# Optimization experiments

Hardware: AMD Instinct MI355X
Metric: run time of the kernel (lower is better)

## Reference

```python
import jax, jax.numpy as jnp
import numpy as np

N = 50000      # nodes
E = 800000     # edges
IN = 128       # in_size
H = 128        # hid_size
OUT = 40       # out_size
L = 3          # num_hid_layers
K = 32         # maxk


def _xavier(key, shape):
    fan_in, fan_out = shape[0], shape[1]
    limit = np.sqrt(6.0 / (fan_in + fan_out))
    return jax.random.uniform(key, shape, jnp.float32, -limit, limit)


def setup_inputs() -> dict:
    key = jax.random.key(0)
    ks = jax.random.split(key, 16)
    x = jax.random.normal(ks[0], (N, IN), jnp.float32)
    src = jax.random.randint(ks[1], (E,), 0, N, jnp.int32)
    dst = jax.random.randint(ks[2], (E,), 0, N, jnp.int32)
    # weights stored as [in, out] so forward is x @ W + b (math-equivalent to torch Linear)
    W_in = _xavier(ks[3], (IN, H)); b_in = jnp.zeros((H,), jnp.float32)
    W_lin = jnp.stack([_xavier(jax.random.fold_in(ks[4], i), (H, H)) for i in range(L)])
    b_lin = jnp.zeros((L, H), jnp.float32)
    W1 = jnp.stack([_xavier(jax.random.fold_in(ks[5], i), (H, H)) for i in range(L)])
    b1 = jnp.zeros((L, H), jnp.float32)
    W2 = jnp.stack([_xavier(jax.random.fold_in(ks[6], i), (H, H)) for i in range(L)])
    b2 = jnp.zeros((L, H), jnp.float32)
    eps = jnp.zeros((L,), jnp.float32)  # learnable eps, init 0
    W_out = _xavier(ks[7], (H, OUT)); b_out = jnp.zeros((OUT,), jnp.float32)
    return {"x": x, "src": src, "dst": dst, "W_in": W_in, "b_in": b_in,
            "W_lin": W_lin, "b_lin": b_lin, "W1": W1, "b1": b1,
            "W2": W2, "b2": b2, "eps": eps, "W_out": W_out, "b_out": b_out}


def _maxk(h, k):
    # keep top-k entries per row, zero the rest (threshold form; ties negligible for random floats)
    thr = jax.lax.top_k(h, k)[0][:, -1:]  # [N, 1] kth-largest value
    return jnp.where(h >= thr, h, 0.0)


def reference(x, src, dst, W_in, b_in, W_lin, b_lin, W1, b1, W2, b2, eps, W_out, b_out):
    h = jax.nn.relu(x @ W_in + b_in)  # [N, H]
    for i in range(L):
        h = h @ W_lin[i] + b_lin[i]
        # GIN conv with MaxK sparsified messages (dropout p=0 / eval mode)
        hs = _maxk(h, K)                                             # [N, H] top-K sparse
        neigh = jax.ops.segment_sum(hs[src], dst, num_segments=N)    # copy_u + sum
        o = (1.0 + eps[i]) * h + neigh
        h = jax.nn.relu(o @ W1[i] + b1[i]) @ W2[i] + b2[i]
    return h @ W_out + b_out  # [N, OUT]
```

## Files before the change

### kernel.cpp

```cpp
#include <hip/hip_runtime.h>

typedef __bf16 bf16x8 __attribute__((ext_vector_type(8)));
typedef float f32x4 __attribute__((ext_vector_type(4)));

__device__ inline unsigned short f2b(float f) {
  unsigned int u = __float_as_uint(f);
  u += 0x7fffu + ((u >> 16) & 1u);
  return (unsigned short)(u >> 16);
}
__device__ inline float b2f(unsigned short u) {
  return __uint_as_float(((unsigned int)u) << 16);
}

__device__ inline int swz(int r, int c) { return r * 128 + (c ^ ((r & 7) << 3)); }

__device__ inline bf16x8 ldfrag(const unsigned short* p) {
  uint4 v = *(const uint4*)p;
  bf16x8 r;
  __builtin_memcpy(&r, &v, 16);
  return r;
}

__global__ __launch_bounds__(256) void prep_wt(
    const float* __restrict__ W_in, const float* __restrict__ W_lin,
    const float* __restrict__ W1, const float* __restrict__ W2,
    const float* __restrict__ W_out, unsigned short* __restrict__ Wh,
    unsigned short* __restrict__ Wl)
{
  int slot = blockIdx.y;
  int e = blockIdx.x * 256 + threadIdx.x;
  int n = e >> 7, k = e & 127;
  const float* srcp; int N;
  if (slot == 0)      { srcp = W_in;                   N = 128; }
  else if (slot < 4)  { srcp = W_lin + (slot-1)*16384; N = 128; }
  else if (slot < 7)  { srcp = W1   + (slot-4)*16384;  N = 128; }
  else if (slot < 10) { srcp = W2   + (slot-7)*16384;  N = 128; }
  else                { srcp = W_out;                  N = 40;  }
  float v = (n < N) ? srcp[k * N + n] : 0.f;
  unsigned short hi = f2b(v);
  float lo = v - b2f(hi);
  Wh[slot * 16384 + e] = hi;
  Wl[slot * 16384 + e] = f2b(lo);
}

template<int WM, int WN, int MF, int NF, int AK, bool RELU>
__global__ __launch_bounds__(256) void gemm_k(
    const float* __restrict__ Ap, const float* __restrict__ neigh,
    const float* __restrict__ epsp, const unsigned short* __restrict__ Wh,
    const unsigned short* __restrict__ Wl, const float* __restrict__ bias,
    float* __restrict__ Cp, int M, int Ncols)
{
  constexpr int BM = WM * MF * 16;
  static_assert(BM * 128 % 1024 == 0, "");
  __shared__ __align__(16) unsigned short ldsAh[BM * 128];
  __shared__ __align__(16) unsigned short ldsAl[BM * 128];

  const int tid = threadIdx.x;
  const int row0 = blockIdx.x * BM;
  float epsf = 0.f;
  if constexpr (AK == 1) epsf = 1.0f + epsp[0];

  constexpr int AIT = BM * 128 / 1024;
#pragma unroll
  for (int it = 0; it < AIT; ++it) {
    int flat = it * 1024 + tid * 4;
    int r = flat >> 7, c = flat & 127;
    int gr = row0 + r;
    float4 v = make_float4(0.f, 0.f, 0.f, 0.f);
    if (gr < M) {
      v = *(const float4*)(Ap + (size_t)gr * 128 + c);
      if constexpr (AK == 1) {
        float4 ng = *(const float4*)(neigh + (size_t)gr * 128 + c);
        v = make_float4(fmaf(epsf, v.x, ng.x), fmaf(epsf, v.y, ng.y),
                        fmaf(epsf, v.z, ng.z), fmaf(epsf, v.w, ng.w));
      }
    }
    ushort4 h4, l4;
    h4.x = f2b(v.x); l4.x = f2b(v.x - b2f(h4.x));
    h4.y = f2b(v.y); l4.y = f2b(v.y - b2f(h4.y));
    h4.z = f2b(v.z); l4.z = f2b(v.z - b2f(h4.z));
    h4.w = f2b(v.w); l4.w = f2b(v.w - b2f(h4.w));
    *(ushort4*)&ldsAh[swz(r, c)] = h4;
    *(ushort4*)&ldsAl[swz(r, c)] = l4;
  }
  __syncthreads();

  const int wid = tid >> 6, lane = tid & 63;
  const int wm = wid / WN, wn = wid % WN;
  const int l15 = lane & 15, lk = lane >> 4;

  f32x4 acc[MF][NF];
#pragma unroll
  for (int mi = 0; mi < MF; ++mi)
#pragma unroll
    for (int ni = 0; ni < NF; ++ni)
      acc[mi][ni] = (f32x4){0.f, 0.f, 0.f, 0.f};

  const unsigned short* wbh = Wh + (size_t)(wn * NF * 16 + l15) * 128;
  const unsigned short* wbl = Wl + (size_t)(wn * NF * 16 + l15) * 128;

#pragma unroll
  for (int kk = 0; kk < 4; ++kk) {
    const int kc = kk * 32 + lk * 8;
    bf16x8 ah[MF], al[MF];
#pragma unroll
    for (int mi = 0; mi < MF; ++mi) {
      int rr = wm * MF * 16 + mi * 16 + l15;
      ah[mi] = ldfrag(&ldsAh[swz(rr, kc)]);
      al[mi] = ldfrag(&ldsAl[swz(rr, kc)]);
    }
    bf16x8 bh[NF], bl[NF];
#pragma unroll
    for (int ni = 0; ni < NF; ++ni) {
      bh[ni] = ldfrag(wbh + ni * 16 * 128 + kc);
      bl[ni] = ldfrag(wbl + ni * 16 * 128 + kc);
    }
#pragma unroll
    for (int mi = 0; mi < MF; ++mi)
#pragma unroll
      for (int ni = 0; ni < NF; ++ni) {
        acc[mi][ni] = __builtin_amdgcn_mfma_f32_16x16x32_bf16(ah[mi], bl[ni], acc[mi][ni], 0, 0, 0);
        acc[mi][ni] = __builtin_amdgcn_mfma_f32_16x16x32_bf16(al[mi], bh[ni], acc[mi][ni], 0, 0, 0);
        acc[mi][ni] = __builtin_amdgcn_mfma_f32_16x16x32_bf16(ah[mi], bh[ni], acc[mi][ni], 0, 0, 0);
      }
  }

#pragma unroll
  for (int ni = 0; ni < NF; ++ni) {
    int col = wn * NF * 16 + ni * 16 + l15;
    if (col >= Ncols) continue;
    float bc = bias[col];
#pragma unroll
    for (int mi = 0; mi < MF; ++mi) {
      int rbase = row0 + wm * MF * 16 + mi * 16 + lk * 4;
#pragma unroll
      for (int j = 0; j < 4; ++j) {
        int r = rbase + j;
        if (r >= M) continue;
        float v = acc[mi][ni][j] + bc;
        if (RELU) v = fmaxf(v, 0.f);
        Cp[(size_t)r * Ncols + col] = v;
      }
    }
  }
}

__global__ __launch_bounds__(256) void maxk_k(const float* __restrict__ h,
                                              float* __restrict__ hs, int M)
{
  int row = blockIdx.x * 4 + (threadIdx.x >> 6);
  if (row >= M) return;
  int lane = threadIdx.x & 63;
  float2 pr = *(const float2*)(h + (size_t)row * 128 + lane * 2);
  auto key = [](float f) -> unsigned int {
    unsigned int b = __float_as_uint(f);
    return (b & 0x80000000u) ? ~b : (b | 0x80000000u);
  };
  unsigned int k0 = key(pr.x), k1 = key(pr.y);
  unsigned int thr = 0;
#pragma unroll
  for (int b = 31; b >= 0; --b) {
    unsigned int t = thr | (1u << b);
    int c = __popcll(__ballot(k0 >= t)) + __popcll(__ballot(k1 >= t));
    if (c >= 32) thr = t;
  }
  unsigned long long g0 = __ballot(k0 > thr), g1 = __ballot(k1 > thr);
  unsigned long long e0 = __ballot(k0 == thr), e1 = __ballot(k1 == thr);
  int cgt = __popcll(g0) + __popcll(g1);
  unsigned long long mlt = (1ull << lane) - 1ull;
  unsigned long long mle = mlt | (1ull << lane);
  bool keep0 = (k0 > thr) ||
               ((k0 == thr) && (cgt + __popcll(e0 & mlt) + __popcll(e1 & mlt)) < 32);
  bool keep1 = (k1 > thr) ||
               ((k1 == thr) && (cgt + __popcll(e0 & mle) + __popcll(e1 & mlt)) < 32);
  float2 o;
  o.x = keep0 ? pr.x : 0.f;
  o.y = keep1 ? pr.y : 0.f;
  *(float2*)(hs + (size_t)row * 128 + lane * 2) = o;
}

__global__ __launch_bounds__(256) void hist_k(const int* __restrict__ dst,
                                              int* __restrict__ cnt, int E)
{
  int e = blockIdx.x * 256 + threadIdx.x;
  if (e < E) atomicAdd(&cnt[dst[e]], 1);
}

__global__ __launch_bounds__(256) void bsum_k(const int* __restrict__ cnt,
                                              int* __restrict__ bsum, int M)
{
  __shared__ int s[256];
  int i = blockIdx.x * 256 + threadIdx.x;
  int t = threadIdx.x;
  s[t] = (i < M) ? cnt[i] : 0;
  __syncthreads();
  for (int st = 128; st > 0; st >>= 1) {
    if (t < st) s[t] += s[t + st];
    __syncthreads();
  }
  if (t == 0) bsum[blockIdx.x] = s[0];
}

__global__ __launch_bounds__(1024) void scanb_k(int* __restrict__ bsum, int NB)
{
  __shared__ int s[1024];
  int t = threadIdx.x;
  int v = (t < NB) ? bsum[t] : 0;
  s[t] = v;
  __syncthreads();
  for (int st = 1; st < 1024; st <<= 1) {
    int a = (t >= st) ? s[t - st] : 0;
    __syncthreads();
    s[t] += a;
    __syncthreads();
  }
  if (t < NB) bsum[t] = s[t] - v;
}

__global__ __launch_bounds__(256) void scano_k(const int* __restrict__ cnt,
                                               const int* __restrict__ bsum,
                                               int* __restrict__ offs,
                                               int* __restrict__ cur, int M, int E)
{
  __shared__ int s[256];
  int i = blockIdx.x * 256 + threadIdx.x;
  int t = threadIdx.x;
  int v = (i < M) ? cnt[i] : 0;
  s[t] = v;
  __syncthreads();
  for (int st = 1; st < 256; st <<= 1) {
    int a = (t >= st) ? s[t - st] : 0;
    __syncthreads();
    s[t] += a;
    __syncthreads();
  }
  int excl = s[t] - v + bsum[blockIdx.x];
  if (i < M) { offs[i] = excl; cur[i] = excl; }
  if (blockIdx.x == 0 && t == 0) offs[M] = E;
}

__global__ __launch_bounds__(256) void fill_k(const int* __restrict__ src,
                                              const int* __restrict__ dst,
                                              int* __restrict__ cur,
                                              unsigned short* __restrict__ eidx, int E)
{
  int e = blockIdx.x * 256 + threadIdx.x;
  if (e >= E) return;
  int d = dst[e];
  int p = atomicAdd(&cur[d], 1);
  eidx[p] = (unsigned short)src[e];
}

__global__ __launch_bounds__(256) void gather_k(
    const float* __restrict__ hs, const int* __restrict__ offs,
    const unsigned short* __restrict__ eidx, float* __restrict__ neigh, int M)
{
  const int w = threadIdx.x >> 6, lane = threadIdx.x & 63;
  const int d = blockIdx.x * 4 + w;
  if (d >= M) return;
  const int start = offs[d], end = offs[d + 1];
  const size_t co = (size_t)lane * 2;
  float ax = 0.f, ay = 0.f;
  int i = start;
  for (; i + 4 <= end; i += 4) {
    int s0 = eidx[i], s1 = eidx[i + 1], s2 = eidx[i + 2], s3 = eidx[i + 3];
    float2 v0 = *(const float2*)(hs + (size_t)s0 * 128 + co);
    float2 v1 = *(const float2*)(hs + (size_t)s1 * 128 + co);
    float2 v2 = *(const float2*)(hs + (size_t)s2 * 128 + co);
    float2 v3 = *(const float2*)(hs + (size_t)s3 * 128 + co);
    ax += (v0.x + v1.x) + (v2.x + v3.x);
    ay += (v0.y + v1.y) + (v2.y + v3.y);
  }
  for (; i < end; ++i) {
    int s0 = eidx[i];
    float2 v0 = *(const float2*)(hs + (size_t)s0 * 128 + co);
    ax += v0.x;
    ay += v0.y;
  }
  float2 o;
  o.x = ax;
  o.y = ay;
  *(float2*)(neigh + (size_t)d * 128 + co) = o;
}

extern "C" void kernel_launch(void* const* d_in, const int* in_sizes, int n_in,
                              void* d_out, int out_size, void* d_ws, size_t ws_size,
                              hipStream_t stream)
{
  const float* x     = (const float*)d_in[0];
  const int*   src   = (const int*)d_in[1];
  const int*   dst   = (const int*)d_in[2];
  const float* W_in  = (const float*)d_in[3];
  const float* b_in  = (const float*)d_in[4];
  const float* W_lin = (const float*)d_in[5];
  const float* b_lin = (const float*)d_in[6];
  const float* W1    = (const float*)d_in[7];
  const float* b1    = (const float*)d_in[8];
  const float* W2    = (const float*)d_in[9];
  const float* b2    = (const float*)d_in[10];
  const float* eps   = (const float*)d_in[11];
  const float* W_out = (const float*)d_in[12];
  const float* b_out = (const float*)d_in[13];

  const int M = in_sizes[0] / 128;
  const int E = in_sizes[1];

  const int NB = (M + 255) / 256;
  char* ws = (char*)d_ws;
  unsigned short* Wh = (unsigned short*)ws;
  size_t off = (size_t)11 * 16384 * 2;
  unsigned short* Wl = (unsigned short*)(ws + off); off += (size_t)11 * 16384 * 2;
  float* PA    = (float*)(ws + off); off += (size_t)M * 128 * 4;
  float* PB    = (float*)(ws + off); off += (size_t)M * 128 * 4;
  float* neigh = (float*)(ws + off); off += (size_t)M * 128 * 4;
  int* offs = (int*)(ws + off); off += (size_t)(M + 1) * 4;
  unsigned short* eidx = (unsigned short*)(ws + off); off += (size_t)E * 2;
  int* cnt  = (int*)(ws + off); off += (size_t)M * 4;
  int* cur  = (int*)(ws + off); off += (size_t)M * 4;
  int* bsum = (int*)(ws + off); off += (size_t)NB * 4;

  dim3 blk(256);
  prep_wt<<<dim3(64, 11), blk, 0, stream>>>(W_in, W_lin, W1, W2, W_out, Wh, Wl);

  (void)hipMemsetAsync(cnt, 0, (size_t)M * 4, stream);
  hist_k<<<(E + 255) / 256, blk, 0, stream>>>(dst, cnt, E);
  bsum_k<<<NB, blk, 0, stream>>>(cnt, bsum, M);
  scanb_k<<<1, 1024, 0, stream>>>(bsum, NB);
  scano_k<<<NB, blk, 0, stream>>>(cnt, bsum, offs, cur, M, E);
  fill_k<<<(E + 255) / 256, blk, 0, stream>>>(src, dst, cur, eidx, E);

  const int gm = (M + 63) / 64;

  float* cur_h = PA;
  float* oth   = PB;
  gemm_k<2,2,2,4,0,true><<<gm, blk, 0, stream>>>(
      x, nullptr, nullptr, Wh, Wl, b_in, cur_h, M, 128);

  for (int i = 0; i < 3; ++i) {
    const size_t ws_off = (size_t)(1 + i) * 16384;
    gemm_k<2,2,2,4,0,false><<<gm, blk, 0, stream>>>(
        cur_h, nullptr, nullptr, Wh + ws_off, Wl + ws_off, b_lin + i * 128, oth, M, 128);
    float* hs = cur_h;
    maxk_k<<<(M + 3) / 4, blk, 0, stream>>>(oth, hs, M);
    gather_k<<<(M + 3) / 4, blk, 0, stream>>>(hs, offs, eidx, neigh, M);
    const size_t w1_off = (size_t)(4 + i) * 16384;
    gemm_k<2,2,2,4,1,true><<<gm, blk, 0, stream>>>(
        oth, neigh, eps + i, Wh + w1_off, Wl + w1_off, b1 + i * 128, cur_h, M, 128);
    const size_t w2_off = (size_t)(7 + i) * 16384;
    gemm_k<2,2,2,4,0,false><<<gm, blk, 0, stream>>>(
        cur_h, nullptr, nullptr, Wh + w2_off, Wl + w2_off, b2 + i * 128, oth, M, 128);
    float* t = cur_h; cur_h = oth; oth = t;
  }

  const size_t wo_off = (size_t)10 * 16384;
  gemm_k<4,1,1,3,0,false><<<gm, blk, 0, stream>>>(
      cur_h, nullptr, nullptr, Wh + wo_off, Wl + wo_off, b_out, (float*)d_out, M, 40);
}
```

Before: 698.8 us.

## Fuse GIN MLP GEMMs and store sparse messages as packed bf16

The two per-layer MLP GEMMs (W1 with ReLU, then W2) become one kernel that keeps the intermediate activation in LDS as hi/lo bf16 splits, so it is never written to and reread from global memory. Separately, maxk now writes the sparsified features as packed bf16 pairs, which halves the bytes the random-access gather reads per edge. The bf16 messages drop the split-precision accuracy that the GEMMs keep, which adds rounding error to the neighbour sums.

```diff
diff --git a/kernel.cpp b/kernel.cpp
--- a/kernel.cpp
+++ b/kernel.cpp
@@ -43,10 +43,9 @@
   Wl[slot * 16384 + e] = f2b(lo);
 }
 
-template<int WM, int WN, int MF, int NF, int AK, bool RELU>
+template<int WM, int WN, int MF, int NF, bool RELU>
 __global__ __launch_bounds__(256) void gemm_k(
-    const float* __restrict__ Ap, const float* __restrict__ neigh,
-    const float* __restrict__ epsp, const unsigned short* __restrict__ Wh,
+    const float* __restrict__ Ap, const unsigned short* __restrict__ Wh,
     const unsigned short* __restrict__ Wl, const float* __restrict__ bias,
     float* __restrict__ Cp, int M, int Ncols)
 {
@@ -57,8 +56,6 @@
 
   const int tid = threadIdx.x;
   const int row0 = blockIdx.x * BM;
-  float epsf = 0.f;
-  if constexpr (AK == 1) epsf = 1.0f + epsp[0];
 
   constexpr int AIT = BM * 128 / 1024;
 #pragma unroll
@@ -67,14 +64,7 @@
     int r = flat >> 7, c = flat & 127;
     int gr = row0 + r;
     float4 v = make_float4(0.f, 0.f, 0.f, 0.f);
-    if (gr < M) {
-      v = *(const float4*)(Ap + (size_t)gr * 128 + c);
-      if constexpr (AK == 1) {
-        float4 ng = *(const float4*)(neigh + (size_t)gr * 128 + c);
-        v = make_float4(fmaf(epsf, v.x, ng.x), fmaf(epsf, v.y, ng.y),
-                        fmaf(epsf, v.z, ng.z), fmaf(epsf, v.w, ng.w));
-      }
-    }
+    if (gr < M) v = *(const float4*)(Ap + (size_t)gr * 128 + c);
     ushort4 h4, l4;
     h4.x = f2b(v.x); l4.x = f2b(v.x - b2f(h4.x));
     h4.y = f2b(v.y); l4.y = f2b(v.y - b2f(h4.y));
@@ -145,8 +135,155 @@
   }
 }
 
+__global__ __launch_bounds__(256) void fusedgemm_k(
+    const float* __restrict__ h2, const float* __restrict__ neigh,
+    const float* __restrict__ epsp,
+    const unsigned short* __restrict__ Wh1, const unsigned short* __restrict__ Wl1,
+    const float* __restrict__ b1,
+    const unsigned short* __restrict__ Wh2, const unsigned short* __restrict__ Wl2,
+    const float* __restrict__ b2, float* __restrict__ Hout, int M)
+{
+  constexpr int WM = 2, WN = 2, MF = 2, NF = 4;
+  constexpr int BM = WM * MF * 16;
+  __shared__ __align__(16) unsigned short ldsAh[BM * 128];
+  __shared__ __align__(16) unsigned short ldsAl[BM * 128];
+
+  const int tid = threadIdx.x;
+  const int row0 = blockIdx.x * BM;
+  const float epsf = 1.0f + epsp[0];
+
+#pragma unroll
+  for (int it = 0; it < BM * 128 / 1024; ++it) {
+    int flat = it * 1024 + tid * 4;
+    int r = flat >> 7, c = flat & 127;
+    int gr = row0 + r;
+    float4 v = make_float4(0.f, 0.f, 0.f, 0.f);
+    if (gr < M) {
+      v = *(const float4*)(h2 + (size_t)gr * 128 + c);
+      float4 ng = *(const float4*)(neigh + (size_t)gr * 128 + c);
+      v = make_float4(fmaf(epsf, v.x, ng.x), fmaf(epsf, v.y, ng.y),
+                      fmaf(epsf, v.z, ng.z), fmaf(epsf, v.w, ng.w));
+    }
+    ushort4 h4, l4;
+    h4.x = f2b(v.x); l4.x = f2b(v.x - b2f(h4.x));
+    h4.y = f2b(v.y); l4.y = f2b(v.y - b2f(h4.y));
+    h4.z = f2b(v.z); l4.z = f2b(v.z - b2f(h4.z));
+    h4.w = f2b(v.w); l4.w = f2b(v.w - b2f(h4.w));
+    *(ushort4*)&ldsAh[swz(r, c)] = h4;
+    *(ushort4*)&ldsAl[swz(r, c)] = l4;
+  }
+  __syncthreads();
+
+  const int wid = tid >> 6, lane = tid & 63;
+  const int wm = wid / WN, wn = wid % WN;
+  const int l15 = lane & 15, lk = lane >> 4;
+
+  f32x4 acc[MF][NF];
+#pragma unroll
+  for (int mi = 0; mi < MF; ++mi)
+#pragma unroll
+    for (int ni = 0; ni < NF; ++ni)
+      acc[mi][ni] = (f32x4){0.f, 0.f, 0.f, 0.f};
+
+  {
+    const unsigned short* wbh = Wh1 + (size_t)(wn * NF * 16 + l15) * 128;
+    const unsigned short* wbl = Wl1 + (size_t)(wn * NF * 16 + l15) * 128;
+#pragma unroll
+    for (int kk = 0; kk < 4; ++kk) {
+      const int kc = kk * 32 + lk * 8;
+      bf16x8 ah[MF], al[MF];
+#pragma unroll
+      for (int mi = 0; mi < MF; ++mi) {
+        int rr = wm * MF * 16 + mi * 16 + l15;
+        ah[mi] = ldfrag(&ldsAh[swz(rr, kc)]);
+        al[mi] = ldfrag(&ldsAl[swz(rr, kc)]);
+      }
+      bf16x8 bh[NF], bl[NF];
+#pragma unroll
+      for (int ni = 0; ni < NF; ++ni) {
+        bh[ni] = ldfrag(wbh + ni * 16 * 128 + kc);
+        bl[ni] = ldfrag(wbl + ni * 16 * 128 + kc);
+      }
+#pragma unroll
+      for (int mi = 0; mi < MF; ++mi)
+#pragma unroll
+        for (int ni = 0; ni < NF; ++ni) {
+          acc[mi][ni] = __builtin_amdgcn_mfma_f32_16x16x32_bf16(ah[mi], bl[ni], acc[mi][ni], 0, 0, 0);
+          acc[mi][ni] = __builtin_amdgcn_mfma_f32_16x16x32_bf16(al[mi], bh[ni], acc[mi][ni], 0, 0, 0);
+          acc[mi][ni] = __builtin_amdgcn_mfma_f32_16x16x32_bf16(ah[mi], bh[ni], acc[mi][ni], 0, 0, 0);
+        }
+    }
+  }
+  __syncthreads();
+
+#pragma unroll
+  for (int ni = 0; ni < NF; ++ni) {
+    int c = wn * NF * 16 + ni * 16 + l15;
+    float bc = b1[c];
+#pragma unroll
+    for (int mi = 0; mi < MF; ++mi) {
+#pragma unroll
+      for (int j = 0; j < 4; ++j) {
+        int r = wm * MF * 16 + mi * 16 + lk * 4 + j;
+        float v = fmaxf(acc[mi][ni][j] + bc, 0.f);
+        unsigned short hi = f2b(v);
+        ldsAh[swz(r, c)] = hi;
+        ldsAl[swz(r, c)] = f2b(v - b2f(hi));
+        acc[mi][ni][j] = 0.f;
+      }
+    }
+  }
+  __syncthreads();
+
+  {
+    const unsigned short* wbh = Wh2 + (size_t)(wn * NF * 16 + l15) * 128;
+    const unsigned short* wbl = Wl2 + (size_t)(wn * NF * 16 + l15) * 128;
+#pragma unroll
+    for (int kk = 0; kk < 4; ++kk) {
+      const int kc = kk * 32 + lk * 8;
+      bf16x8 ah[MF], al[MF];
+#pragma unroll
+      for (int mi = 0; mi < MF; ++mi) {
+        int rr = wm * MF * 16 + mi * 16 + l15;
+        ah[mi] = ldfrag(&ldsAh[swz(rr, kc)]);
+        al[mi] = ldfrag(&ldsAl[swz(rr, kc)]);
+      }
+      bf16x8 bh[NF], bl[NF];
+#pragma unroll
+      for (int ni = 0; ni < NF; ++ni) {
+        bh[ni] = ldfrag(wbh + ni * 16 * 128 + kc);
+        bl[ni] = ldfrag(wbl + ni * 16 * 128 + kc);
+      }
+#pragma unroll
+      for (int mi = 0; mi < MF; ++mi)
+#pragma unroll
+        for (int ni = 0; ni < NF; ++ni) {
+          acc[mi][ni] = __builtin_amdgcn_mfma_f32_16x16x32_bf16(ah[mi], bl[ni], acc[mi][ni], 0, 0, 0);
+          acc[mi][ni] = __builtin_amdgcn_mfma_f32_16x16x32_bf16(al[mi], bh[ni], acc[mi][ni], 0, 0, 0);
+          acc[mi][ni] = __builtin_amdgcn_mfma_f32_16x16x32_bf16(ah[mi], bh[ni], acc[mi][ni], 0, 0, 0);
+        }
+    }
+  }
+
+#pragma unroll
+  for (int ni = 0; ni < NF; ++ni) {
+    int col = wn * NF * 16 + ni * 16 + l15;
+    float bc = b2[col];
+#pragma unroll
+    for (int mi = 0; mi < MF; ++mi) {
+      int rbase = row0 + wm * MF * 16 + mi * 16 + lk * 4;
+#pragma unroll
+      for (int j = 0; j < 4; ++j) {
+        int r = rbase + j;
+        if (r >= M) continue;
+        Hout[(size_t)r * 128 + col] = acc[mi][ni][j] + bc;
+      }
+    }
+  }
+}
+
 __global__ __launch_bounds__(256) void maxk_k(const float* __restrict__ h,
-                                              float* __restrict__ hs, int M)
+                                              unsigned int* __restrict__ hs, int M)
 {
   int row = blockIdx.x * 4 + (threadIdx.x >> 6);
   if (row >= M) return;
@@ -173,10 +310,9 @@
                ((k0 == thr) && (cgt + __popcll(e0 & mlt) + __popcll(e1 & mlt)) < 32);
   bool keep1 = (k1 > thr) ||
                ((k1 == thr) && (cgt + __popcll(e0 & mle) + __popcll(e1 & mlt)) < 32);
-  float2 o;
-  o.x = keep0 ? pr.x : 0.f;
-  o.y = keep1 ? pr.y : 0.f;
-  *(float2*)(hs + (size_t)row * 128 + lane * 2) = o;
+  unsigned int w0 = keep0 ? (unsigned int)f2b(pr.x) : 0u;
+  unsigned int w1 = keep1 ? (unsigned int)f2b(pr.y) : 0u;
+  hs[(size_t)row * 64 + lane] = w0 | (w1 << 16);
 }
 
 __global__ __launch_bounds__(256) void hist_k(const int* __restrict__ dst,
@@ -252,35 +388,34 @@
 }
 
 __global__ __launch_bounds__(256) void gather_k(
-    const float* __restrict__ hs, const int* __restrict__ offs,
+    const unsigned int* __restrict__ hs, const int* __restrict__ offs,
     const unsigned short* __restrict__ eidx, float* __restrict__ neigh, int M)
 {
   const int w = threadIdx.x >> 6, lane = threadIdx.x & 63;
   const int d = blockIdx.x * 4 + w;
   if (d >= M) return;
   const int start = offs[d], end = offs[d + 1];
-  const size_t co = (size_t)lane * 2;
   float ax = 0.f, ay = 0.f;
   int i = start;
   for (; i + 4 <= end; i += 4) {
     int s0 = eidx[i], s1 = eidx[i + 1], s2 = eidx[i + 2], s3 = eidx[i + 3];
-    float2 v0 = *(const float2*)(hs + (size_t)s0 * 128 + co);
-    float2 v1 = *(const float2*)(hs + (size_t)s1 * 128 + co);
-    float2 v2 = *(const float2*)(hs + (size_t)s2 * 128 + co);
-    float2 v3 = *(const float2*)(hs + (size_t)s3 * 128 + co);
-    ax += (v0.x + v1.x) + (v2.x + v3.x);
-    ay += (v0.y + v1.y) + (v2.y + v3.y);
+    unsigned int u0 = hs[(size_t)s0 * 64 + lane];
+    unsigned int u1 = hs[(size_t)s1 * 64 + lane];
+    unsigned int u2 = hs[(size_t)s2 * 64 + lane];
+    unsigned int u3 = hs[(size_t)s3 * 64 + lane];
+    ax += (b2f(u0 & 0xffffu) + b2f(u1 & 0xffffu)) +
+          (b2f(u2 & 0xffffu) + b2f(u3 & 0xffffu));
+    ay += (b2f(u0 >> 16) + b2f(u1 >> 16)) + (b2f(u2 >> 16) + b2f(u3 >> 16));
   }
   for (; i < end; ++i) {
-    int s0 = eidx[i];
-    float2 v0 = *(const float2*)(hs + (size_t)s0 * 128 + co);
-    ax += v0.x;
-    ay += v0.y;
+    unsigned int u0 = hs[(size_t)eidx[i] * 64 + lane];
+    ax += b2f(u0 & 0xffffu);
+    ay += b2f(u0 >> 16);
   }
   float2 o;
   o.x = ax;
   o.y = ay;
-  *(float2*)(neigh + (size_t)d * 128 + co) = o;
+  *(float2*)(neigh + (size_t)d * 128 + (size_t)lane * 2) = o;
 }
 
 extern "C" void kernel_launch(void* const* d_in, const int* in_sizes, int n_in,
@@ -331,28 +466,26 @@
 
   const int gm = (M + 63) / 64;
 
-  float* cur_h = PA;
-  float* oth   = PB;
-  gemm_k<2,2,2,4,0,true><<<gm, blk, 0, stream>>>(
-      x, nullptr, nullptr, Wh, Wl, b_in, cur_h, M, 128);
+  float* hbuf = PA;
+  float* h2buf = PB;
+  gemm_k<2,2,2,4,true><<<gm, blk, 0, stream>>>(
+      x, Wh, Wl, b_in, hbuf, M, 128);
 
   for (int i = 0; i < 3; ++i) {
-    const size_t ws_off = (size_t)(1 + i) * 16384;
-    gemm_k<2,2,2,4,0,false><<<gm, blk, 0, stream>>>(
-        cur_h, nullptr, nullptr, Wh + ws_off, Wl + ws_off, b_lin + i * 128, oth, M, 128);
-    float* hs = cur_h;
-    maxk_k<<<(M + 3) / 4, blk, 0, stream>>>(oth, hs, M);
+    const size_t wlin_off = (size_t)(1 + i) * 16384;
+    const size_t w1_off   = (size_t)(4 + i) * 16384;
+    const size_t w2_off   = (size_t)(7 + i) * 16384;
+    gemm_k<2,2,2,4,false><<<gm, blk, 0, stream>>>(
+        hbuf, Wh + wlin_off, Wl + wlin_off, b_lin + i * 128, h2buf, M, 128);
+    unsigned int* hs = (unsigned int*)hbuf;
+    maxk_k<<<(M + 3) / 4, blk, 0, stream>>>(h2buf, hs, M);
     gather_k<<<(M + 3) / 4, blk, 0, stream>>>(hs, offs, eidx, neigh, M);
-    const size_t w1_off = (size_t)(4 + i) * 16384;
-    gemm_k<2,2,2,4,1,true><<<gm, blk, 0, stream>>>(
-        oth, neigh, eps + i, Wh + w1_off, Wl + w1_off, b1 + i * 128, cur_h, M, 128);
-    const size_t w2_off = (size_t)(7 + i) * 16384;
-    gemm_k<2,2,2,4,0,false><<<gm, blk, 0, stream>>>(
-        cur_h, nullptr, nullptr, Wh + w2_off, Wl + w2_off, b2 + i * 128, oth, M, 128);
-    float* t = cur_h; cur_h = oth; oth = t;
+    fusedgemm_k<<<gm, blk, 0, stream>>>(
+        h2buf, neigh, eps + i, Wh + w1_off, Wl + w1_off, b1 + i * 128,
+        Wh + w2_off, Wl + w2_off, b2 + i * 128, hbuf, M);
   }
 
   const size_t wo_off = (size_t)10 * 16384;
-  gemm_k<4,1,1,3,0,false><<<gm, blk, 0, stream>>>(
-      cur_h, nullptr, nullptr, Wh + wo_off, Wl + wo_off, b_out, (float*)d_out, M, 40);
-}
+  gemm_k<4,1,1,3,false><<<gm, blk, 0, stream>>>(
+      hbuf, Wh + wo_off, Wl + wo_off, b_out, (float*)d_out, M, 40);
+}
```

After: 627.4 us. 1.11x faster.
